# Kernel tuning notes

Measured on AMD Instinct MI355X. Metric: run time of the kernel, lower is better.

The kernel has to match this reference:

```python
import math
import jax, jax.numpy as jnp
import numpy as np

D_MODEL = 1024
N_HEADS = 16
D_HEAD = D_MODEL // N_HEADS
ROPE_BASE = 10000.0
MAX_SEQ_LEN = 2048


def build_cos_sin_cache(d_head, max_seq_len, base=ROPE_BASE):
    half = d_head // 2
    i = jnp.arange(half, dtype=jnp.float32)
    theta = 1.0 / (base ** (2.0 * i / d_head))  # (half,)
    t = jnp.arange(max_seq_len, dtype=jnp.float32)
    angles = jnp.outer(t, theta)  # (T, half)
    return jnp.cos(angles), jnp.sin(angles)


def rotate_half(x):
    d = x.shape[-1]
    x1, x2 = x[..., : d // 2], x[..., d // 2 :]
    return jnp.concatenate([-x2, x1], axis=-1)


def apply_rope(x, cos_t, sin_t):
    # x: (..., T, d_head); cos_t/sin_t: (T, d_head//2)
    cos_full = jnp.concatenate([cos_t, cos_t], axis=-1)
    sin_full = jnp.concatenate([sin_t, sin_t], axis=-1)
    return x * cos_full + rotate_half(x) * sin_full


def setup_inputs() -> dict:
    key = jax.random.key(0)
    ks = jax.random.split(key, 5)
    B, T = 2, 2048
    s = 1.0 / math.sqrt(D_MODEL)
    return {
        "x": jax.random.normal(ks[0], (B, T, D_MODEL), dtype=jnp.float32),
        "Wq": jax.random.normal(ks[1], (D_MODEL, D_MODEL), dtype=jnp.float32) * s,
        "Wk": jax.random.normal(ks[2], (D_MODEL, D_MODEL), dtype=jnp.float32) * s,
        "Wv": jax.random.normal(ks[3], (D_MODEL, D_MODEL), dtype=jnp.float32) * s,
        "Wo": jax.random.normal(ks[4], (D_MODEL, D_MODEL), dtype=jnp.float32) * s,
    }


def reference(x, Wq, Wk, Wv, Wo):
    B, T, _ = x.shape
    # Linear with torch weight convention: y = x @ W.T
    q = jnp.einsum("btd,ed->bte", x, Wq)
    k = jnp.einsum("btd,ed->bte", x, Wk)
    v = jnp.einsum("btd,ed->bte", x, Wv)
    # (B, H, T, d_head)
    q = q.reshape(B, T, N_HEADS, D_HEAD).transpose(0, 2, 1, 3)
    k = k.reshape(B, T, N_HEADS, D_HEAD).transpose(0, 2, 1, 3)
    v = v.reshape(B, T, N_HEADS, D_HEAD).transpose(0, 2, 1, 3)
    cos_c, sin_c = build_cos_sin_cache(D_HEAD, MAX_SEQ_LEN)
    cos_t, sin_t = cos_c[:T], sin_c[:T]
    q = apply_rope(q, cos_t, sin_t)
    k = apply_rope(k, cos_t, sin_t)
    scale = math.sqrt(D_HEAD)
    scores = jnp.einsum("bhqd,bhkd->bhqk", q, k) / scale
    causal = jnp.triu(jnp.full((T, T), -jnp.inf, dtype=x.dtype), k=1)
    scores = scores + causal
    weights = jax.nn.softmax(scores, axis=-1)
    out = jnp.einsum("bhqk,bhkd->bhqd", weights, v)
    out = out.transpose(0, 2, 1, 3).reshape(B, T, D_MODEL)
    return jnp.einsum("btd,ed->bte", out, Wo)
```

## Files before the change

kernel.cpp:

```cpp
#include <hip/hip_runtime.h>
#include <stdint.h>
#include <math.h>

typedef __attribute__((ext_vector_type(8))) short short8;
typedef __attribute__((ext_vector_type(4))) float f32x4;
typedef __attribute__((ext_vector_type(16))) float f32x16;

#define T_SEQ 2048
#define MROWS 4096
#define LOG2E 1.44269504088896f

#define OFF_XBF   ((size_t)0)
#define OFF_WQ    ((size_t)8388608)
#define OFF_WK    ((size_t)10485760)
#define OFF_WV    ((size_t)12582912)
#define OFF_WO    ((size_t)14680064)
#define OFF_Q     ((size_t)16777216)
#define OFF_K     ((size_t)25165824)
#define OFF_VT    ((size_t)33554432)
#define OFF_ATT   ((size_t)41943040)
#define OFF_COS   ((size_t)50331648)
#define OFF_SIN   ((size_t)50593792)
#define OFF_OPART ((size_t)0)
#define OFF_ML    ((size_t)8388608)

__device__ __forceinline__ unsigned short f2bf(float f) {
  unsigned u = __float_as_uint(f);
  u += 0x7fffu + ((u >> 16) & 1u);
  return (unsigned short)(u >> 16);
}

__device__ __forceinline__ float bf2f(unsigned short u) {
  return __uint_as_float((unsigned)u << 16);
}

__device__ __forceinline__ void gld_lds16(const void* g, void* l) {
  __builtin_amdgcn_global_load_lds(
      (__attribute__((address_space(1))) void*)(g),
      (__attribute__((address_space(3))) void*)(l), 16, 0, 0);
}

__device__ __forceinline__ unsigned cvt_pk_bf16(float lo, float hi) {
  unsigned r;
  asm("v_cvt_pk_bf16_f32 %0, %1, %2" : "=v"(r) : "v"(lo), "v"(hi));
  return r;
}

__global__ void prep_kernel(const float* x, const float* wq, const float* wk,
                            const float* wv, const float* wo, char* ws) {
  const size_t NX4 = (size_t)MROWS * 1024 / 4;
  const size_t NW4 = (size_t)1024 * 1024 / 4;
  const size_t NT = (size_t)T_SEQ * 32;
  unsigned short* xb = (unsigned short*)(ws + OFF_XBF);
  unsigned short* wqb = (unsigned short*)(ws + OFF_WQ);
  unsigned short* wkb = (unsigned short*)(ws + OFF_WK);
  unsigned short* wvb = (unsigned short*)(ws + OFF_WV);
  unsigned short* wob = (unsigned short*)(ws + OFF_WO);
  float* cosb = (float*)(ws + OFF_COS);
  float* sinb = (float*)(ws + OFF_SIN);
  size_t nvec = NX4 + 4 * NW4;
  size_t total = nvec + NT;
  for (size_t i = (size_t)blockIdx.x * blockDim.x + threadIdx.x; i < total;
       i += (size_t)gridDim.x * blockDim.x) {
    if (i < nvec) {
      const float* src;
      unsigned short* dst;
      size_t e;
      if (i < NX4) {
        src = x; dst = xb; e = i * 4;
      } else {
        size_t j = i - NX4;
        int wsel = (int)(j / NW4);
        e = (j - (size_t)wsel * NW4) * 4;
        src = wsel == 0 ? wq : wsel == 1 ? wk : wsel == 2 ? wv : wo;
        dst = wsel == 0 ? wqb : wsel == 1 ? wkb : wsel == 2 ? wvb : wob;
      }
      float4 v = *(const float4*)(src + e);
      unsigned long long p =
          (unsigned long long)f2bf(v.x) |
          ((unsigned long long)f2bf(v.y) << 16) |
          ((unsigned long long)f2bf(v.z) << 32) |
          ((unsigned long long)f2bf(v.w) << 48);
      *(unsigned long long*)(dst + e) = p;
    } else {
      size_t j = i - nvec;
      int t = (int)(j >> 5), ii = (int)(j & 31);
      double th = exp(-(double)ii * (9.210340371976184 / 32.0));
      float ang = (float)t * (float)th;
      cosb[j] = cosf(ang);
      sinb[j] = sinf(ang);
    }
  }
}

__global__ __launch_bounds__(256, 2) void gemm_qkv(
    const unsigned short* Abf, const unsigned short* Wall, unsigned short* qkout,
    unsigned short* vtout, const float* cosT, const float* sinT) {
  const int K = 1024;
  int bid = blockIdx.x;
  int bm = bid / 24, bn = bid % 24;
  int sel = bn >> 3, bnc = bn & 7;
  int tid = threadIdx.x;
  int l = tid & 63, w = tid >> 6;
  int wm = w >> 1, wn = w & 1;
  int g = l >> 4;

  __shared__ __align__(16) char ldsbuf[32768];

  auto stage = [&](int kt, int buf) {
    int base = buf * 16384;
#pragma unroll
    for (int i = 0; i < 2; ++i) {
      int p = (w * 2 + i) * 1024;
      int row = (p >> 6) + (l >> 2);
      int u = l & 3;
      const char* ga = (const char*)Abf +
          ((size_t)(bm * 128 + row) * K + (size_t)kt * 32) * 2 + u * 16;
      gld_lds16(ga, ldsbuf + base + p);
      const char* gb = (const char*)Wall +
          ((size_t)(bn * 128 + row) * K + (size_t)kt * 32) * 2 + u * 16;
      gld_lds16(gb, ldsbuf + base + 8192 + p);
    }
  };

  f32x4 acc[4][4] = {};
  stage(0, 0);
  const int nk = K / 32;
  for (int kt = 0; kt < nk; ++kt) {
    int buf = kt & 1;
    __syncthreads();
    if (kt + 1 < nk) stage(kt + 1, buf ^ 1);
    const char* Ab = ldsbuf + buf * 16384;
    const char* Bb = Ab + 8192;
    short8 af[4], bfr[4];
#pragma unroll
    for (int m = 0; m < 4; ++m)
      af[m] = *(const short8*)(Ab + (wm * 64 + m * 16 + (l & 15)) * 64 + g * 16);
#pragma unroll
    for (int n = 0; n < 4; ++n)
      bfr[n] = *(const short8*)(Bb + (wn * 64 + n * 16 + (l & 15)) * 64 + g * 16);
#pragma unroll
    for (int m = 0; m < 4; ++m)
#pragma unroll
      for (int n = 0; n < 4; ++n)
        acc[m][n] = __builtin_amdgcn_mfma_f32_16x16x32_bf16(af[m], bfr[n],
                                                            acc[m][n], 0, 0, 0);
    __syncthreads();
  }

  int row0 = bm * 128 + wm * 64;
  int col0 = bnc * 128 + wn * 64;
  if (sel < 2) {
    float qscale = sel == 0 ? 0.125f * LOG2E : 1.0f;
    unsigned short* C = qkout + (size_t)sel * MROWS * 1024;
#pragma unroll
    for (int m = 0; m < 4; ++m)
#pragma unroll
      for (int n = 0; n < 2; ++n)
#pragma unroll
        for (int r = 0; r < 4; ++r) {
          int row = row0 + m * 16 + g * 4 + r;
          int t = row & (T_SEQ - 1);
          int d = n * 16 + (l & 15);
          float c = cosT[t * 32 + d], s = sinT[t * 32 + d];
          float v0 = acc[m][n][r], v1 = acc[m][n + 2][r];
          C[(size_t)row * 1024 + col0 + d] = f2bf((v0 * c - v1 * s) * qscale);
          C[(size_t)row * 1024 + col0 + d + 32] = f2bf((v1 * c + v0 * s) * qscale);
        }
  } else {
    unsigned short* C = vtout;
#pragma unroll
    for (int m = 0; m < 4; ++m) {
      int rowb = row0 + m * 16 + g * 4;
      int bb = rowb >> 11, t0 = rowb & (T_SEQ - 1);
#pragma unroll
      for (int n = 0; n < 4; ++n) {
        int e = col0 + n * 16 + (l & 15);
        unsigned long long pv =
            (unsigned long long)f2bf(acc[m][n][0]) |
            ((unsigned long long)f2bf(acc[m][n][1]) << 16) |
            ((unsigned long long)f2bf(acc[m][n][2]) << 32) |
            ((unsigned long long)f2bf(acc[m][n][3]) << 48);
        *(unsigned long long*)(C + ((size_t)bb * 1024 + e) * T_SEQ + t0) = pv;
      }
    }
  }
}

__global__ __launch_bounds__(256, 2) void gemm_wo(const unsigned short* Abf,
                                                  const unsigned short* Wbf,
                                                  float* out) {
  const int K = 1024, N = 1024;
  int bid = blockIdx.x;
  int bm = bid >> 3, bn = bid & 7;
  int tid = threadIdx.x;
  int l = tid & 63, w = tid >> 6;
  int wm = w >> 1, wn = w & 1;
  int g = l >> 4;

  __shared__ __align__(16) char ldsbuf[32768];

  auto stage = [&](int kt, int buf) {
    int base = buf * 16384;
#pragma unroll
    for (int i = 0; i < 2; ++i) {
      int p = (w * 2 + i) * 1024;
      int row = (p >> 6) + (l >> 2);
      int u = l & 3;
      const char* ga = (const char*)Abf +
          ((size_t)(bm * 128 + row) * K + (size_t)kt * 32) * 2 + u * 16;
      gld_lds16(ga, ldsbuf + base + p);
      const char* gb = (const char*)Wbf +
          ((size_t)(bn * 128 + row) * K + (size_t)kt * 32) * 2 + u * 16;
      gld_lds16(gb, ldsbuf + base + 8192 + p);
    }
  };

  f32x4 acc[4][4] = {};
  stage(0, 0);
  const int nk = K / 32;
  for (int kt = 0; kt < nk; ++kt) {
    int buf = kt & 1;
    __syncthreads();
    if (kt + 1 < nk) stage(kt + 1, buf ^ 1);
    const char* Ab = ldsbuf + buf * 16384;
    const char* Bb = Ab + 8192;
    short8 af[4], bfr[4];
#pragma unroll
    for (int m = 0; m < 4; ++m)
      af[m] = *(const short8*)(Ab + (wm * 64 + m * 16 + (l & 15)) * 64 + g * 16);
#pragma unroll
    for (int n = 0; n < 4; ++n)
      bfr[n] = *(const short8*)(Bb + (wn * 64 + n * 16 + (l & 15)) * 64 + g * 16);
#pragma unroll
    for (int m = 0; m < 4; ++m)
#pragma unroll
      for (int n = 0; n < 4; ++n)
        acc[m][n] = __builtin_amdgcn_mfma_f32_16x16x32_bf16(af[m], bfr[n],
                                                            acc[m][n], 0, 0, 0);
    __syncthreads();
  }

  int row0 = bm * 128 + wm * 64;
  int col0 = bn * 128 + wn * 64;
#pragma unroll
  for (int m = 0; m < 4; ++m)
#pragma unroll
    for (int n = 0; n < 4; ++n)
#pragma unroll
      for (int r = 0; r < 4; ++r)
        out[(size_t)(row0 + m * 16 + g * 4 + r) * N + col0 + n * 16 + (l & 15)] =
            acc[m][n][r];
}

__global__ __launch_bounds__(256, 3) void attn_kernel(
    const unsigned short* Qbf, const unsigned short* Kbf,
    const unsigned short* VT, unsigned short* att,
    unsigned short* Opart, float* mlpart) {
  int bid = blockIdx.x;
  int band = bid >> 8;
  int c = bid & 255;
  int bh = c & 31;
  int a = c >> 5;
  int b = bh >> 4, h = bh & 15;
  int qt, kt0, ntt, s;
  if (band == 2) {
    qt = a; s = 0; kt0 = 0; ntt = 2 * qt + 2;
  } else {
    qt = 15 - a; s = band;
    int ht = qt + 1;
    kt0 = s * ht; ntt = ht;
  }
  int tid = threadIdx.x;
  int l = tid & 63, w = tid >> 6;
  int q32 = l & 31, hi = l >> 5;
  int q0 = qt * 128;
  int q0w = q0 + w * 32;
  int ntw = ((q0w + 95) >> 6) - kt0;
  if (ntw > ntt) ntw = ntt;

  __shared__ __align__(16) char lds[2][16384];

  short8 qf[4];
  {
    const char* qb = (const char*)Qbf +
        ((size_t)(b * T_SEQ + q0w + q32)) * 2048 + h * 128 + hi * 16;
#pragma unroll
    for (int ks = 0; ks < 4; ++ks) qf[ks] = *(const short8*)(qb + ks * 32);
  }
  asm volatile("s_waitcnt vmcnt(0)" ::: "memory");

  auto stage = [&](int gt, int buf) {
    char* Kd = &lds[buf][0];
    char* Vd = &lds[buf][8192];
    int row = tid >> 3;
    int colb = (tid & 7) * 16;
#pragma unroll
    for (int r = 0; r < 2; ++r) {
      int d = row + r * 32;
      int sc = colb ^ ((d & 7) << 4);
      const char* gk = (const char*)Kbf +
          ((size_t)(b * T_SEQ + gt * 64 + d)) * 2048 + h * 128 + sc;
      gld_lds16(gk, Kd + d * 128 + colb);
      const char* gv = (const char*)VT +
          ((size_t)(b * 1024 + h * 64 + d)) * 4096 + gt * 128 + sc;
      gld_lds16(gv, Vd + d * 128 + colb);
    }
  };

  f32x16 o0 = {}, o1 = {};
  float m_run = -1e30f, l_run = 0.f;
  stage(kt0, 0);
  for (int kt = 0; kt < ntt; ++kt) {
    int buf = kt & 1;
    if (kt + 1 < ntt) {
      stage(kt0 + kt + 1, buf ^ 1);
      asm volatile("s_waitcnt vmcnt(4)" ::: "memory");
    } else {
      asm volatile("s_waitcnt vmcnt(0)" ::: "memory");
    }
    __builtin_amdgcn_s_barrier();
    __builtin_amdgcn_sched_barrier(0);
    if (kt < ntw) {
      int gt = kt0 + kt;
      const char* Kl = &lds[buf][0];
      const char* Vl = &lds[buf][8192];

      f32x16 st0 = {}, st1 = {};
      __builtin_amdgcn_s_setprio(1);
#pragma unroll
      for (int ks = 0; ks < 4; ++ks) {
        int sc = (ks * 32 + hi * 16) ^ ((q32 & 7) << 4);
        short8 k0 = *(const short8*)(Kl + q32 * 128 + sc);
        short8 k1 = *(const short8*)(Kl + (q32 + 32) * 128 + sc);
        st0 = __builtin_amdgcn_mfma_f32_32x32x16_bf16(k0, qf[ks], st0, 0, 0, 0);
        st1 = __builtin_amdgcn_mfma_f32_32x32x16_bf16(k1, qf[ks], st1, 0, 0, 0);
      }
      __builtin_amdgcn_s_setprio(0);

      if (gt * 64 + 63 > q0w) {
        int qa = q0w + q32;
#pragma unroll
        for (int r = 0; r < 16; ++r) {
          int kkb = gt * 64 + (r & 3) + 8 * (r >> 2) + 4 * hi;
          if (kkb > qa) st0[r] = -1e30f;
          if (kkb + 32 > qa) st1[r] = -1e30f;
        }
      }

      float tm = -1e30f;
#pragma unroll
      for (int r = 0; r < 16; ++r) {
        tm = fmaxf(tm, st0[r]);
        tm = fmaxf(tm, st1[r]);
      }
      tm = fmaxf(tm, __shfl_xor(tm, 32));
      if (__any(tm > m_run)) {
        float m_new = fmaxf(m_run, tm);
        float fac = exp2f(m_run - m_new);
        l_run *= fac;
#pragma unroll
        for (int r = 0; r < 16; ++r) {
          o0[r] *= fac;
          o1[r] *= fac;
        }
        m_run = m_new;
      }
      float ls = 0.f;
#pragma unroll
      for (int r = 0; r < 16; ++r) {
        st0[r] = exp2f(st0[r] - m_run);
        st1[r] = exp2f(st1[r] - m_run);
        ls += st0[r] + st1[r];
      }
      ls += __shfl_xor(ls, 32);
      l_run += ls;

      short8 pb[4];
#pragma unroll
      for (int ks = 0; ks < 4; ++ks) {
        union { unsigned u[4]; short8 s8; } uu;
#pragma unroll
        for (int j = 0; j < 4; ++j) {
          int bse = (ks & 1) * 8 + 2 * j;
          float aa = (ks & 2) ? st1[bse] : st0[bse];
          float cc = (ks & 2) ? st1[bse + 1] : st0[bse + 1];
          uu.u[j] = cvt_pk_bf16(aa, cc);
        }
        pb[ks] = uu.s8;
      }

      __builtin_amdgcn_s_setprio(1);
#pragma unroll
      for (int ks = 0; ks < 4; ++ks) {
        int sp = (q32 & 7) << 4;
        int cA = (ks * 32 + 8 * hi) ^ sp;
        int cB = (ks * 32 + 16 + 8 * hi) ^ sp;
#pragma unroll
        for (int cc = 0; cc < 2; ++cc) {
          int dv = cc * 32 + q32;
          union { unsigned long long u[2]; short8 s8; } vv;
          vv.u[0] = *(const unsigned long long*)(Vl + dv * 128 + cA);
          vv.u[1] = *(const unsigned long long*)(Vl + dv * 128 + cB);
          if (cc == 0)
            o0 = __builtin_amdgcn_mfma_f32_32x32x16_bf16(vv.s8, pb[ks], o0, 0, 0, 0);
          else
            o1 = __builtin_amdgcn_mfma_f32_32x32x16_bf16(vv.s8, pb[ks], o1, 0, 0, 0);
        }
      }
      __builtin_amdgcn_s_setprio(0);
    }
    __builtin_amdgcn_s_barrier();
  }

  float scale = (band == 2) ? (1.0f / l_run) : 1.0f;
  if (band != 2 && hi == 0) {
    float2 ml = {m_run, l_run};
    int pbi = ((bh << 3) + (qt - 8)) * 2 + s;
    *(float2*)(mlpart + ((size_t)pbi * 128 + w * 32 + q32) * 2) = ml;
  }
  __syncthreads();
  float* Ol = (float*)lds;
#pragma unroll
  for (int cc = 0; cc < 2; ++cc)
#pragma unroll
    for (int r = 0; r < 16; ++r) {
      int d = cc * 32 + (r & 3) + 8 * (r >> 2) + 4 * hi;
      float v = (cc ? o1[r] : o0[r]) * scale;
      Ol[w * 2048 + q32 * 64 + (d ^ (q32 & 31))] = v;
    }
  __syncthreads();
#pragma unroll
  for (int i = 0; i < 4; ++i) {
    int idx2 = tid + i * 256;
    int row = idx2 >> 3;
    int seg = idx2 & 7;
    int q = row & 31, wq = row >> 5;
    unsigned short tmp[8];
#pragma unroll
    for (int j = 0; j < 8; ++j) {
      int d = seg * 8 + j;
      tmp[j] = f2bf(Ol[wq * 2048 + q * 64 + (d ^ (q & 31))]);
    }
    if (band == 2) {
      *(unsigned long long*)(att + ((size_t)(b * T_SEQ + q0 + row)) * 1024 +
                             h * 64 + seg * 8) = *(unsigned long long*)&tmp[0];
      *(unsigned long long*)(att + ((size_t)(b * T_SEQ + q0 + row)) * 1024 +
                             h * 64 + seg * 8 + 4) = *(unsigned long long*)&tmp[4];
    } else {
      int pbi = ((bh << 3) + (qt - 8)) * 2 + s;
      *(unsigned long long*)(Opart + ((size_t)pbi * 128 + row) * 64 + seg * 8) =
          *(unsigned long long*)&tmp[0];
      *(unsigned long long*)(Opart + ((size_t)pbi * 128 + row) * 64 + seg * 8 + 4) =
          *(unsigned long long*)&tmp[4];
    }
  }
}

__global__ __launch_bounds__(256) void combine_kernel(
    const unsigned short* Opart, const float* mlpart, unsigned short* att) {
  int blk = blockIdx.x;
  int bh = blk >> 3, j = blk & 7;
  int b = bh >> 4, h = bh & 15;
  int q0 = (8 + j) * 128;
  int pb0 = ((bh << 3) + j) * 2;
  const unsigned short* O0 = Opart + (size_t)pb0 * 128 * 64;
  const unsigned short* O1 = O0 + 128 * 64;
  const float* ml0 = mlpart + (size_t)pb0 * 256;
  const float* ml1 = ml0 + 256;
#pragma unroll
  for (int i = 0; i < 4; ++i) {
    int u = threadIdx.x + i * 256;
    int q = u >> 3, seg = u & 7;
    float m0 = ml0[q * 2], l0 = ml0[q * 2 + 1];
    float m1 = ml1[q * 2], l1 = ml1[q * 2 + 1];
    float m = fmaxf(m0, m1);
    float e0 = exp2f(m0 - m), e1 = exp2f(m1 - m);
    float inv = 1.0f / (l0 * e0 + l1 * e1);
    float s0 = e0 * inv, s1 = e1 * inv;
    short8 a = *(const short8*)(O0 + (size_t)q * 64 + seg * 8);
    short8 cvec = *(const short8*)(O1 + (size_t)q * 64 + seg * 8);
    union { unsigned short us[8]; short8 s8; } ov;
#pragma unroll
    for (int k = 0; k < 8; ++k)
      ov.us[k] = f2bf(bf2f((unsigned short)a[k]) * s0 +
                      bf2f((unsigned short)cvec[k]) * s1);
    *(short8*)(att + ((size_t)(b * T_SEQ + q0 + q)) * 1024 + h * 64 + seg * 8) =
        ov.s8;
  }
}

extern "C" void kernel_launch(void* const* d_in, const int* in_sizes, int n_in,
                              void* d_out, int out_size, void* d_ws,
                              size_t ws_size, hipStream_t stream) {
  const float* x = (const float*)d_in[0];
  const float* Wq = (const float*)d_in[1];
  const float* Wk = (const float*)d_in[2];
  const float* Wv = (const float*)d_in[3];
  const float* Wo = (const float*)d_in[4];
  char* ws = (char*)d_ws;

  unsigned short* xb = (unsigned short*)(ws + OFF_XBF);
  unsigned short* wall = (unsigned short*)(ws + OFF_WQ);
  unsigned short* wob = (unsigned short*)(ws + OFF_WO);
  unsigned short* qbf = (unsigned short*)(ws + OFF_Q);
  unsigned short* vtb = (unsigned short*)(ws + OFF_VT);
  unsigned short* att = (unsigned short*)(ws + OFF_ATT);
  unsigned short* kbf = (unsigned short*)(ws + OFF_K);
  unsigned short* opart = (unsigned short*)(ws + OFF_OPART);
  float* mlp = (float*)(ws + OFF_ML);
  const float* cosT = (const float*)(ws + OFF_COS);
  const float* sinT = (const float*)(ws + OFF_SIN);

  prep_kernel<<<2048, 256, 0, stream>>>(x, Wq, Wk, Wv, Wo, ws);
  gemm_qkv<<<768, 256, 0, stream>>>(xb, wall, qbf, vtb, cosT, sinT);
  attn_kernel<<<768, 256, 0, stream>>>(qbf, kbf, vtb, att, opart, mlp);
  combine_kernel<<<256, 256, 0, stream>>>(opart, mlp, att);
  gemm_wo<<<256, 256, 0, stream>>>(att, wob, (float*)d_out);
}
```

Baseline: 115.5 us.

## Rebalance causal attention split-KV partitioning with variable splits and remapped block order

Replaces the fixed two-band split-KV scheme with a per-query-tile split count (1, 2 or 3 splits depending on tile length) and a static remap table that orders blocks so the longest work is dispatched first. The attention grid grows from 768 to 960 blocks, the combine kernel generalises to merge up to three partials, and the occupancy hint rises to four blocks per CU. The aim is to cut tail imbalance in the causal attention. The cost is more partial-output traffic and combine work, plus extra register pressure from the higher occupancy target.

```diff
diff --git a/kernel.cpp b/kernel.cpp
--- a/kernel.cpp
+++ b/kernel.cpp
@@ -22,7 +22,7 @@
 #define OFF_COS   ((size_t)50331648)
 #define OFF_SIN   ((size_t)50593792)
 #define OFF_OPART ((size_t)0)
-#define OFF_ML    ((size_t)8388608)
+#define OFF_ML    ((size_t)12582912)
 
 __device__ __forceinline__ unsigned short f2bf(float f) {
   unsigned u = __float_as_uint(f);
@@ -253,24 +253,30 @@
             acc[m][n][r];
 }
 
-__global__ __launch_bounds__(256, 3) void attn_kernel(
+__global__ __launch_bounds__(256, 4) void attn_kernel(
     const unsigned short* Qbf, const unsigned short* Kbf,
     const unsigned short* VT, unsigned short* att,
     unsigned short* Opart, float* mlpart) {
+  static const unsigned char remap[30] = {
+      5, 16, 17, 14, 15, 28, 29, 4, 12, 13, 23, 24, 25, 26, 27,
+      10, 11, 19, 20, 21, 22, 3, 8, 9, 18, 6, 7, 2, 1, 0};
   int bid = blockIdx.x;
-  int band = bid >> 8;
-  int c = bid & 255;
-  int bh = c & 31;
-  int a = c >> 5;
+  int bh = bid & 31;
+  int cid = remap[bid >> 5];
   int b = bh >> 4, h = bh & 15;
-  int qt, kt0, ntt, s;
-  if (band == 2) {
-    qt = a; s = 0; kt0 = 0; ntt = 2 * qt + 2;
+  int qt, s, ns;
+  if (cid < 6) {
+    qt = cid; s = 0; ns = 1;
+  } else if (cid < 18) {
+    int e = cid - 6; qt = 6 + (e >> 1); s = e & 1; ns = 2;
   } else {
-    qt = 15 - a; s = band;
-    int ht = qt + 1;
-    kt0 = s * ht; ntt = ht;
-  }
+    int e = cid - 18; qt = 12 + e / 3; s = e - 3 * (e / 3); ns = 3;
+  }
+  int ntt_full = 2 * qt + 2;
+  int kt0 = (s * ntt_full) / ns;
+  int ntt = ((s + 1) * ntt_full) / ns - kt0;
+  int pbi = bh * 24 + (ns == 2 ? (cid - 6) : (cid - 18 + 12));
+
   int tid = threadIdx.x;
   int l = tid & 63, w = tid >> 6;
   int q32 = l & 31, hi = l >> 5;
@@ -278,6 +284,7 @@
   int q0w = q0 + w * 32;
   int ntw = ((q0w + 95) >> 6) - kt0;
   if (ntw > ntt) ntw = ntt;
+  if (ntw < 0) ntw = 0;
 
   __shared__ __align__(16) char lds[2][16384];
 
@@ -413,10 +420,9 @@
     __builtin_amdgcn_s_barrier();
   }
 
-  float scale = (band == 2) ? (1.0f / l_run) : 1.0f;
-  if (band != 2 && hi == 0) {
+  float scale = (ns == 1) ? (1.0f / l_run) : 1.0f;
+  if (ns > 1 && hi == 0) {
     float2 ml = {m_run, l_run};
-    int pbi = ((bh << 3) + (qt - 8)) * 2 + s;
     *(float2*)(mlpart + ((size_t)pbi * 128 + w * 32 + q32) * 2) = ml;
   }
   __syncthreads();
@@ -442,13 +448,12 @@
       int d = seg * 8 + j;
       tmp[j] = f2bf(Ol[wq * 2048 + q * 64 + (d ^ (q & 31))]);
     }
-    if (band == 2) {
+    if (ns == 1) {
       *(unsigned long long*)(att + ((size_t)(b * T_SEQ + q0 + row)) * 1024 +
                              h * 64 + seg * 8) = *(unsigned long long*)&tmp[0];
       *(unsigned long long*)(att + ((size_t)(b * T_SEQ + q0 + row)) * 1024 +
                              h * 64 + seg * 8 + 4) = *(unsigned long long*)&tmp[4];
     } else {
-      int pbi = ((bh << 3) + (qt - 8)) * 2 + s;
       *(unsigned long long*)(Opart + ((size_t)pbi * 128 + row) * 64 + seg * 8) =
           *(unsigned long long*)&tmp[0];
       *(unsigned long long*)(Opart + ((size_t)pbi * 128 + row) * 64 + seg * 8 + 4) =
@@ -460,33 +465,54 @@
 __global__ __launch_bounds__(256) void combine_kernel(
     const unsigned short* Opart, const float* mlpart, unsigned short* att) {
   int blk = blockIdx.x;
-  int bh = blk >> 3, j = blk & 7;
+  int bh = blk & 31, j = blk >> 5;
+  int qt = 6 + j;
   int b = bh >> 4, h = bh & 15;
-  int q0 = (8 + j) * 128;
-  int pb0 = ((bh << 3) + j) * 2;
-  const unsigned short* O0 = Opart + (size_t)pb0 * 128 * 64;
-  const unsigned short* O1 = O0 + 128 * 64;
-  const float* ml0 = mlpart + (size_t)pb0 * 256;
-  const float* ml1 = ml0 + 256;
+  int q0 = qt * 128;
+  int ns = qt < 12 ? 2 : 3;
+  int base = qt < 12 ? (qt - 6) * 2 : 12 + (qt - 12) * 3;
+  int pbi0 = bh * 24 + base;
 #pragma unroll
   for (int i = 0; i < 4; ++i) {
     int u = threadIdx.x + i * 256;
     int q = u >> 3, seg = u & 7;
-    float m0 = ml0[q * 2], l0 = ml0[q * 2 + 1];
-    float m1 = ml1[q * 2], l1 = ml1[q * 2 + 1];
-    float m = fmaxf(m0, m1);
-    float e0 = exp2f(m0 - m), e1 = exp2f(m1 - m);
-    float inv = 1.0f / (l0 * e0 + l1 * e1);
-    float s0 = e0 * inv, s1 = e1 * inv;
-    short8 a = *(const short8*)(O0 + (size_t)q * 64 + seg * 8);
-    short8 cvec = *(const short8*)(O1 + (size_t)q * 64 + seg * 8);
-    union { unsigned short us[8]; short8 s8; } ov;
-#pragma unroll
-    for (int k = 0; k < 8; ++k)
-      ov.us[k] = f2bf(bf2f((unsigned short)a[k]) * s0 +
-                      bf2f((unsigned short)cvec[k]) * s1);
+    float m = -1e30f;
+    float mp[3], lp[3];
+#pragma unroll
+    for (int p = 0; p < 3; ++p) {
+      if (p < ns) {
+        mp[p] = mlpart[((size_t)(pbi0 + p) * 128 + q) * 2];
+        lp[p] = mlpart[((size_t)(pbi0 + p) * 128 + q) * 2 + 1];
+        m = fmaxf(m, mp[p]);
+      }
+    }
+    float denom = 0.f;
+    float sp[3];
+#pragma unroll
+    for (int p = 0; p < 3; ++p) {
+      if (p < ns) {
+        sp[p] = exp2f(mp[p] - m);
+        denom += lp[p] * sp[p];
+      }
+    }
+    float inv = 1.0f / denom;
+    float accv[8] = {};
+#pragma unroll
+    for (int p = 0; p < 3; ++p) {
+      if (p < ns) {
+        float w = sp[p] * inv;
+        short8 ov = *(const short8*)(Opart +
+            ((size_t)(pbi0 + p) * 128 + q) * 64 + seg * 8);
+#pragma unroll
+        for (int k = 0; k < 8; ++k)
+          accv[k] += bf2f((unsigned short)ov[k]) * w;
+      }
+    }
+    union { unsigned short us[8]; short8 s8; } r;
+#pragma unroll
+    for (int k = 0; k < 8; ++k) r.us[k] = f2bf(accv[k]);
     *(short8*)(att + ((size_t)(b * T_SEQ + q0 + q)) * 1024 + h * 64 + seg * 8) =
-        ov.s8;
+        r.s8;
   }
 }
 
@@ -514,7 +540,7 @@
 
   prep_kernel<<<2048, 256, 0, stream>>>(x, Wq, Wk, Wv, Wo, ws);
   gemm_qkv<<<768, 256, 0, stream>>>(xb, wall, qbf, vtb, cosT, sinT);
-  attn_kernel<<<768, 256, 0, stream>>>(qbf, kbf, vtb, att, opart, mlp);
-  combine_kernel<<<256, 256, 0, stream>>>(opart, mlp, att);
+  attn_kernel<<<960, 256, 0, stream>>>(qbf, kbf, vtb, att, opart, mlp);
+  combine_kernel<<<320, 256, 0, stream>>>(opart, mlp, att);
   gemm_wo<<<256, 256, 0, stream>>>(att, wob, (float*)d_out);
 }
```

New measurement: 116.7 us. No clear change (+1.1%).
